# Optimization experiments

Measured on AMD Instinct MI355X. Metric: run time of the kernel, lower is better.

## Reference

```python
import jax, jax.numpy as jnp
import numpy as np

N_NODES = 100000
N_EDGES = 1600000
D = 128          # h_size == feature_representation_size
N_CLASSES = 2
N_GRAPHS = 64


def setup_inputs() -> dict:
    key = jax.random.key(0)
    ks = jax.random.split(key, 8)
    scale = 1.0 / np.sqrt(D)
    x = jax.random.normal(ks[0], (N_NODES, D), jnp.float32)
    edge_index = jax.random.randint(ks[1], (2, N_EDGES), 0, N_NODES, dtype=jnp.int64)
    batch = jnp.sort(jax.random.randint(ks[2], (N_NODES,), 0, N_GRAPHS, dtype=jnp.int64))
    W0 = jax.random.normal(ks[3], (D, D), jnp.float32) * scale
    W1 = jax.random.normal(ks[4], (D, D), jnp.float32) * scale
    W2 = jax.random.normal(ks[5], (D, D), jnp.float32) * scale
    Wf = jax.random.normal(ks[6], (D, N_CLASSES), jnp.float32) * scale
    return dict(
        x=x, edge_index=edge_index, batch=batch,
        W0=W0, b0=jnp.zeros((D,), jnp.float32),
        W1=W1, b1=jnp.zeros((D,), jnp.float32),
        W2=W2, b2=jnp.zeros((D,), jnp.float32),
        Wf=Wf, bf=jnp.zeros((N_CLASSES,), jnp.float32),
    )


def gcn_norm(edge_index, num_nodes):
    # add self loops, symmetric normalization D^{-1/2} A_hat D^{-1/2}
    src, dst = edge_index[0], edge_index[1]
    loop = jnp.arange(num_nodes, dtype=src.dtype)
    src = jnp.concatenate([src, loop])
    dst = jnp.concatenate([dst, loop])
    ew = jnp.ones(src.shape[0], jnp.float32)
    deg = jax.ops.segment_sum(ew, dst, num_segments=num_nodes)
    dinv = jnp.where(deg > 0, jax.lax.rsqrt(deg), 0.0)
    norm = dinv[src] * dinv[dst]  # [E+N]
    return src, dst, norm


def gcn_conv(h, W, b, src, dst, norm, num_nodes):
    h = h @ W                                   # linear transform
    msg = h[src] * norm[:, None]                # gather + scale over edges
    out = jax.ops.segment_sum(msg, dst, num_segments=num_nodes)  # scatter-add
    return out + b


def reference(x, edge_index, batch, W0, b0, W1, b1, W2, b2, Wf, bf):
    n = x.shape[0]
    src, dst, norm = gcn_norm(edge_index, n)
    h = jax.nn.relu(gcn_conv(x, W0, b0, src, dst, norm, n))
    h = jax.nn.relu(gcn_conv(h, W1, b1, src, dst, norm, n))
    h = gcn_conv(h, W2, b2, src, dst, norm, n)  # last layer, no relu
    pooled = jax.ops.segment_max(h, batch, num_segments=N_GRAPHS)  # global max pool
    return pooled @ Wf + bf
```

## Files before the change

### kernel.cpp

```cpp
#include <hip/hip_runtime.h>
#include <hip/hip_bf16.h>
#include <hip/hip_fp16.h>
#include <float.h>

#define D 128
#define NGRAPHS 64
#define BKSHIFT 9
#define BKNODES 512
#define MAXBK 256
#define PCH 2048

typedef _Float16 h8 __attribute__((ext_vector_type(8)));
typedef float f4 __attribute__((ext_vector_type(4)));

__device__ __forceinline__ unsigned fkey(float f){
  unsigned u = __float_as_uint(f);
  return (u & 0x80000000u) ? ~u : (u | 0x80000000u);
}
__device__ __forceinline__ float funkey(unsigned k){
  unsigned u = (k & 0x80000000u) ? (k ^ 0x80000000u) : ~k;
  return __uint_as_float(u);
}

__device__ __forceinline__ void wcvt_pair(const float* __restrict__ W,
    _Float16* __restrict__ dstp, int pair, int lane){
  int quad = lane >> 4;
  int n    = lane & 15;
  int k0 = pair >> 3;
  int tt = pair & 7;
  _Float16 v[8];
  #pragma unroll
  for (int j = 0; j < 8; j++){
    int k = k0 * 32 + quad * 8 + j;
    v[j] = (_Float16)W[k * 128 + 16 * tt + n];
  }
  *(uint4*)&dstp[((size_t)pair * 64 + lane) * 8] = *(uint4*)v;
}

__global__ __launch_bounds__(256) void k_wcvt0(const float* __restrict__ W0,
    _Float16* __restrict__ Wsw, int* __restrict__ bcnt){
  if (blockIdx.x == 0 && threadIdx.x < MAXBK) bcnt[threadIdx.x] = 0;
  int lane = threadIdx.x & 63;
  int pair = blockIdx.x * 4 + (threadIdx.x >> 6);
  wcvt_pair(W0, Wsw, pair, lane);
}

#define HCH 4096
__global__ __launch_bounds__(256) void k_mega(
    const float* __restrict__ x, const _Float16* __restrict__ Wsw0,
    _Float16* __restrict__ C, int M, int gb,
    const int* __restrict__ dst, int* __restrict__ bcnt, int E, int nh,
    const float* __restrict__ W1, const float* __restrict__ W2,
    _Float16* __restrict__ Wsw12){
  __shared__ __align__(16) char smraw[4 * 16 * 136 * 2];
  int bid = blockIdx.x;
  if (bid < gb){
    _Float16 (*lds)[136] = (_Float16(*)[136])(smraw + (threadIdx.x >> 6) * 16 * 136 * 2);
    int lane = threadIdx.x & 63;
    int quad = lane >> 4;
    int l15  = lane & 15;
    int m0 = bid * 64 + (threadIdx.x >> 6) * 16;
    if (m0 >= M) return;
    f4 acc[8] = {};
    h8 af[4];
    const float* arow = x + (size_t)(m0 + l15) * D;
    #pragma unroll
    for (int k0 = 0; k0 < 4; k0++){
      float4 a = *(const float4*)&arow[k0 * 32 + quad * 8];
      float4 b = *(const float4*)&arow[k0 * 32 + quad * 8 + 4];
      __half2 p0 = __floats2half2_rn(a.x, a.y);
      __half2 p1 = __floats2half2_rn(a.z, a.w);
      __half2 p2 = __floats2half2_rn(b.x, b.y);
      __half2 p3 = __floats2half2_rn(b.z, b.w);
      union { uint4 u; h8 v; } cv;
      cv.u.x = *(unsigned*)&p0; cv.u.y = *(unsigned*)&p1;
      cv.u.z = *(unsigned*)&p2; cv.u.w = *(unsigned*)&p3;
      af[k0] = cv.v;
    }
    #pragma unroll
    for (int k0 = 0; k0 < 4; k0++){
      #pragma unroll
      for (int t = 0; t < 8; t++){
        h8 bf = *(const h8*)&Wsw0[((size_t)(k0 * 8 + t) * 64 + lane) * 8];
        acc[t] = __builtin_amdgcn_mfma_f32_16x16x32_f16(af[k0], bf, acc[t], 0, 0, 0);
      }
    }
    #pragma unroll
    for (int t = 0; t < 8; t++){
      #pragma unroll
      for (int r = 0; r < 4; r++)
        lds[quad * 4 + r][t * 16 + l15] = (_Float16)acc[t][r];
    }
    #pragma unroll
    for (int it = 0; it < 4; it++){
      int idx = it * 64 + lane;
      int row = idx >> 4;
      int ch  = idx & 15;
      *(uint4*)&C[(size_t)(m0 + row) * D + ch * 8] = *(uint4*)&lds[row][ch * 8];
    }
    return;
  }
  bid -= gb;
  if (bid < nh){
    int* h = (int*)smraw;
    int t = threadIdx.x;
    for (int i = t; i < MAXBK; i += 256) h[i] = 0;
    __syncthreads();
    int e0 = bid * HCH;
    #pragma unroll
    for (int j = 0; j < HCH / 256; j++){
      int e = e0 + t + j * 256;
      if (e < E) atomicAdd(&h[dst[e] >> BKSHIFT], 1);
    }
    __syncthreads();
    for (int i = t; i < MAXBK; i += 256) if (h[i]) atomicAdd(&bcnt[i], h[i]);
    return;
  }
  bid -= nh;
  const float* W = (bid < 2) ? W1 : W2;
  _Float16* dstp = Wsw12 + ((bid < 2) ? 0 : 16384);
  int pbase = (bid & 1) * 16;
  int lane = threadIdx.x & 63;
  for (int pp = (threadIdx.x >> 6); pp < 16; pp += 4)
    wcvt_pair(W, dstp, pbase + pp, lane);
}

__global__ __launch_bounds__(256) void k_bscan(const int* __restrict__ bcnt,
    int* __restrict__ bOff, int* __restrict__ bCur, int* __restrict__ row_ptr,
    unsigned* __restrict__ pk, int nbk, int N, int E){
  __shared__ int sh[256];
  int t = threadIdx.x;
  for (int i = t; i < NGRAPHS * D; i += 256) pk[i] = 0u;
  int v = (t < nbk) ? bcnt[t] : 0;
  sh[t] = v; __syncthreads();
  for (int off = 1; off < 256; off <<= 1){
    int x = (t >= off) ? sh[t - off] : 0;
    __syncthreads();
    sh[t] += x;
    __syncthreads();
  }
  if (t < nbk){ int ex = sh[t] - v; bOff[t] = ex; bCur[t] = ex; }
  if (t == 0){ bOff[nbk] = E; row_ptr[N] = E; }
}

__global__ __launch_bounds__(256) void k_part(const int* __restrict__ src,
    const int* __restrict__ dst, int* __restrict__ bCur,
    uint2* __restrict__ epart, int E){
  __shared__ int scnt[MAXBK], soff[MAXBK], sbase[MAXBK], scur[MAXBK];
  __shared__ int stmp[256];
  __shared__ uint2 stage[PCH];
  int t = threadIdx.x;
  int e0 = blockIdx.x * PCH;
  int eN = E - e0; if (eN > PCH) eN = PCH;
  for (int i = t; i < MAXBK; i += 256){ scnt[i] = 0; scur[i] = 0; }
  __syncthreads();
  uint2 mye[PCH / 256];
  #pragma unroll
  for (int j = 0; j < PCH / 256; j++){
    int e = e0 + t + j * 256;
    if (e < E){
      mye[j].x = (unsigned)src[e];
      mye[j].y = (unsigned)dst[e];
      atomicAdd(&scnt[mye[j].y >> BKSHIFT], 1);
    }
  }
  __syncthreads();
  int v = scnt[t];
  stmp[t] = v; __syncthreads();
  for (int off = 1; off < 256; off <<= 1){
    int x = (t >= off) ? stmp[t - off] : 0;
    __syncthreads();
    stmp[t] += x;
    __syncthreads();
  }
  soff[t] = stmp[t] - v;
  if (v > 0) sbase[t] = atomicAdd(&bCur[t], v);
  __syncthreads();
  #pragma unroll
  for (int j = 0; j < PCH / 256; j++){
    int e = e0 + t + j * 256;
    if (e < E){
      int b = mye[j].y >> BKSHIFT;
      int l = atomicAdd(&scur[b], 1);
      stage[soff[b] + l] = mye[j];
    }
  }
  __syncthreads();
  for (int j = t; j < eN; j += 256){
    uint2 ed = stage[j];
    int b = (int)(ed.y >> BKSHIFT);
    epart[(size_t)sbase[b] + (j - soff[b])] = ed;
  }
}

__global__ __launch_bounds__(256) void k_bfill(const uint2* __restrict__ epart,
    const int* __restrict__ bOff, int* __restrict__ row_ptr,
    int* __restrict__ col, float* __restrict__ dinv, int N){
  __shared__ int hc[BKNODES], off[BKNODES], cur[BKNODES];
  __shared__ int stmp[256];
  int b = blockIdx.x, t = threadIdx.x;
  int base = bOff[b], cntE = bOff[b + 1] - base;
  int node0 = b << BKSHIFT;
  int nloc = N - node0; if (nloc > BKNODES) nloc = BKNODES;
  for (int i = t; i < BKNODES; i += 256) hc[i] = 0;
  __syncthreads();
  for (int j = t; j < cntE; j += 256){
    uint2 ed = epart[(size_t)base + j];
    atomicAdd(&hc[ed.y - node0], 1);
  }
  __syncthreads();
  int a0 = hc[2 * t], a1 = hc[2 * t + 1];
  int s = a0 + a1;
  stmp[t] = s; __syncthreads();
  for (int o = 1; o < 256; o <<= 1){
    int x = (t >= o) ? stmp[t - o] : 0;
    __syncthreads();
    stmp[t] += x;
    __syncthreads();
  }
  int ex = stmp[t] - s;
  off[2 * t] = ex; off[2 * t + 1] = ex + a0;
  __syncthreads();
  for (int i = t; i < nloc; i += 256){
    row_ptr[node0 + i] = base + off[i];
    dinv[node0 + i]    = rsqrtf((float)hc[i] + 1.0f);
    cur[i] = off[i];
  }
  __syncthreads();
  for (int j = t; j < cntE; j += 256){
    uint2 ed = epart[(size_t)base + j];
    int p = atomicAdd(&cur[ed.y - node0], 1);
    col[base + p] = (int)ed.x;
  }
}

__global__ __launch_bounds__(256) void gemm_mfma(const _Float16* __restrict__ A,
    const _Float16* __restrict__ Wsw, _Float16* __restrict__ C, int M){
  __shared__ _Float16 lds[4][16][136];
  int wave = threadIdx.x >> 6;
  int lane = threadIdx.x & 63;
  int quad = lane >> 4;
  int l15  = lane & 15;
  int m0 = blockIdx.x * 64 + wave * 16;
  if (m0 >= M) return;
  f4 acc[8] = {};
  h8 af[4];
  const _Float16* arow = A + (size_t)(m0 + l15) * D;
  #pragma unroll
  for (int k0 = 0; k0 < 4; k0++)
    af[k0] = *(const h8*)&arow[k0 * 32 + quad * 8];
  #pragma unroll
  for (int k0 = 0; k0 < 4; k0++){
    #pragma unroll
    for (int t = 0; t < 8; t++){
      h8 bf = *(const h8*)&Wsw[((size_t)(k0 * 8 + t) * 64 + lane) * 8];
      acc[t] = __builtin_amdgcn_mfma_f32_16x16x32_f16(af[k0], bf, acc[t], 0, 0, 0);
    }
  }
  #pragma unroll
  for (int t = 0; t < 8; t++){
    #pragma unroll
    for (int r = 0; r < 4; r++)
      lds[wave][quad * 4 + r][t * 16 + l15] = (_Float16)acc[t][r];
  }
  #pragma unroll
  for (int it = 0; it < 4; it++){
    int idx = it * 64 + lane;
    int row = idx >> 4;
    int ch  = idx & 15;
    *(uint4*)&C[(size_t)(m0 + row) * D + ch * 8] = *(uint4*)&lds[wave][row][ch * 8];
  }
}

__device__ __forceinline__ void accm(float* acc, uint4 u, float w){
  union { uint4 u; _Float16 h[8]; } cv;
  cv.u = u;
  #pragma unroll
  for (int k = 0; k < 8; k++)
    acc[k] += (float)cv.h[k] * w;
}

__global__ __launch_bounds__(256) void k_agg(const __half* __restrict__ t,
    const int* __restrict__ row_ptr, const int* __restrict__ col,
    const float* __restrict__ dinv, const float* __restrict__ bias,
    __half* __restrict__ outh, int relu, int N){
  int node = blockIdx.x * 4 + (threadIdx.x >> 6);
  if (node >= N) return;
  int lane = threadIdx.x & 63;
  int way  = lane >> 4;
  int cg   = (lane & 15) * 8;
  float di = dinv[node];
  int beg = row_ptr[node], end = row_ptr[node + 1];
  float acc[8] = {0.f,0.f,0.f,0.f,0.f,0.f,0.f,0.f};
  int j = beg + way;
  for (; j + 12 < end; j += 16){
    int s0 = col[j], s1 = col[j + 4], s2 = col[j + 8], s3 = col[j + 12];
    float w0 = dinv[s0] * di;
    float w1 = dinv[s1] * di;
    float w2 = dinv[s2] * di;
    float w3 = dinv[s3] * di;
    uint4 u0 = *(const uint4*)&t[(size_t)s0 * D + cg];
    uint4 u1 = *(const uint4*)&t[(size_t)s1 * D + cg];
    uint4 u2 = *(const uint4*)&t[(size_t)s2 * D + cg];
    uint4 u3 = *(const uint4*)&t[(size_t)s3 * D + cg];
    accm(acc, u0, w0);
    accm(acc, u1, w1);
    accm(acc, u2, w2);
    accm(acc, u3, w3);
  }
  for (; j < end; j += 4){
    int s = col[j];
    float w = dinv[s] * di;
    uint4 u = *(const uint4*)&t[(size_t)s * D + cg];
    accm(acc, u, w);
  }
  #pragma unroll
  for (int k = 0; k < 8; k++){
    acc[k] += __shfl_xor(acc[k], 16, 64);
    acc[k] += __shfl_xor(acc[k], 32, 64);
  }
  if (way == 0){
    uint4 su = *(const uint4*)&t[(size_t)node * D + cg];
    union { uint4 u; _Float16 h[8]; } sv; sv.u = su;
    float dii = di * di;
    float4 b0 = *(const float4*)&bias[cg];
    float4 b1 = *(const float4*)&bias[cg + 4];
    float bb[8] = {b0.x, b0.y, b0.z, b0.w, b1.x, b1.y, b1.z, b1.w};
    float o[8];
    #pragma unroll
    for (int k = 0; k < 8; k++)
      o[k] = acc[k] + (float)sv.h[k] * dii + bb[k];
    if (relu){
      #pragma unroll
      for (int k = 0; k < 8; k++) o[k] = fmaxf(o[k], 0.f);
    }
    __half2 p0 = __floats2half2_rn(o[0], o[1]);
    __half2 p1 = __floats2half2_rn(o[2], o[3]);
    __half2 p2 = __floats2half2_rn(o[4], o[5]);
    __half2 p3 = __floats2half2_rn(o[6], o[7]);
    uint4 u;
    u.x = *(unsigned*)&p0; u.y = *(unsigned*)&p1;
    u.z = *(unsigned*)&p2; u.w = *(unsigned*)&p3;
    *(uint4*)&outh[(size_t)node * D + cg] = u;
  }
}

__global__ __launch_bounds__(128) void k_pool(const __half* __restrict__ h,
    const int* __restrict__ batch, unsigned* __restrict__ pk, int N){
  int d = threadIdx.x;
  int n0 = blockIdx.x * 64;
  int nEnd = n0 + 64; if (nEnd > N) nEnd = N;
  float cur = -FLT_MAX;
  int curg = batch[n0];
  int n = n0;
  for (; n + 3 < nEnd; n += 4){
    const __half* r = &h[(size_t)n * D + d];
    __half v0 = r[0], v1 = r[D], v2 = r[2 * D], v3 = r[3 * D];
    int g0 = batch[n], g1 = batch[n + 1], g2 = batch[n + 2], g3 = batch[n + 3];
    if (g0 != curg){ atomicMax(&pk[curg * D + d], fkey(cur)); cur = -FLT_MAX; curg = g0; }
    cur = fmaxf(cur, __half2float(v0));
    if (g1 != curg){ atomicMax(&pk[curg * D + d], fkey(cur)); cur = -FLT_MAX; curg = g1; }
    cur = fmaxf(cur, __half2float(v1));
    if (g2 != curg){ atomicMax(&pk[curg * D + d], fkey(cur)); cur = -FLT_MAX; curg = g2; }
    cur = fmaxf(cur, __half2float(v2));
    if (g3 != curg){ atomicMax(&pk[curg * D + d], fkey(cur)); cur = -FLT_MAX; curg = g3; }
    cur = fmaxf(cur, __half2float(v3));
  }
  for (; n < nEnd; n++){
    int g = batch[n];
    if (g != curg){ atomicMax(&pk[curg * D + d], fkey(cur)); cur = -FLT_MAX; curg = g; }
    cur = fmaxf(cur, __half2float(h[(size_t)n * D + d]));
  }
  atomicMax(&pk[curg * D + d], fkey(cur));
}

__global__ __launch_bounds__(128) void k_final(const unsigned* __restrict__ pk,
    const float* __restrict__ Wf, const float* __restrict__ bf,
    float* __restrict__ out){
  int t = threadIdx.x;
  int g = t >> 1, c = t & 1;
  float s = bf[c];
  for (int k = 0; k < D; k++)
    s += funkey(pk[g * D + k]) * Wf[k * 2 + c];
  out[g * 2 + c] = s;
}

extern "C" void kernel_launch(void* const* d_in, const int* in_sizes, int n_in,
                              void* d_out, int out_size, void* d_ws, size_t ws_size,
                              hipStream_t stream){
  const float* x   = (const float*)d_in[0];
  const int*   ei  = (const int*)d_in[1];
  const int*   bat = (const int*)d_in[2];
  const float* W0  = (const float*)d_in[3];
  const float* b0  = (const float*)d_in[4];
  const float* W1  = (const float*)d_in[5];
  const float* b1  = (const float*)d_in[6];
  const float* W2  = (const float*)d_in[7];
  const float* b2  = (const float*)d_in[8];
  const float* Wf  = (const float*)d_in[9];
  const float* bf  = (const float*)d_in[10];
  int N = in_sizes[0] / D;
  int E = in_sizes[1] / 2;
  const int* srcp = ei;
  const int* dstp = ei + E;
  int nbk   = (N + BKNODES - 1) / BKNODES;
  int npart = (E + PCH - 1) / PCH;
  int nh    = (E + HCH - 1) / HCH;
  int gb    = (N + 63) / 64;

  char* p = (char*)d_ws;
  auto alloc = [&](size_t bytes)->char*{
    char* r = p; p += (bytes + 255) & ~(size_t)255; return r;
  };
  float*     dinv    = (float*)alloc((size_t)N * 4);
  int*       row_ptr = (int*)alloc((size_t)(N + 1) * 4);
  int*       col     = (int*)alloc((size_t)E * 4);
  uint2*     epart   = (uint2*)alloc((size_t)E * 8);
  _Float16*  tmp     = (_Float16*)alloc((size_t)N * D * 2);
  _Float16*  tmp2    = (_Float16*)alloc((size_t)N * D * 2);
  _Float16*  Wsw     = (_Float16*)alloc((size_t)3 * 16384 * 2);
  unsigned*  pk      = (unsigned*)alloc((size_t)NGRAPHS * D * 4);
  int*       bcnt    = (int*)alloc((size_t)MAXBK * 4);
  int*       bOff    = (int*)alloc((size_t)(MAXBK + 1) * 4);
  int*       bCur    = (int*)alloc((size_t)MAXBK * 4);

  k_wcvt0<<<8, 256, 0, stream>>>(W0, Wsw, bcnt);
  k_mega<<<gb + nh + 4, 256, 0, stream>>>(x, Wsw, tmp, N, gb,
      dstp, bcnt, E, nh, W1, W2, Wsw + 16384);
  k_bscan<<<1, 256, 0, stream>>>(bcnt, bOff, bCur, row_ptr, pk, nbk, N, E);
  k_part<<<npart, 256, 0, stream>>>(srcp, dstp, bCur, epart, E);
  k_bfill<<<nbk, 256, 0, stream>>>(epart, bOff, row_ptr, col, dinv, N);

  int ablocks = (N + 3) / 4;
  k_agg<<<ablocks, 256, 0, stream>>>((const __half*)tmp, row_ptr, col, dinv, b0, (__half*)tmp2, 1, N);
  gemm_mfma<<<gb, 256, 0, stream>>>(tmp2, Wsw + 16384, tmp, N);
  k_agg<<<ablocks, 256, 0, stream>>>((const __half*)tmp, row_ptr, col, dinv, b1, (__half*)tmp2, 1, N);
  gemm_mfma<<<gb, 256, 0, stream>>>(tmp2, Wsw + 32768, tmp, N);
  k_agg<<<ablocks, 256, 0, stream>>>((const __half*)tmp, row_ptr, col, dinv, b2, (__half*)tmp2, 0, N);
  k_pool<<<(N + 63) / 64, 128, 0, stream>>>((const __half*)tmp2, bat, pk, N);
  k_final<<<1, 128, 0, stream>>>(pk, Wf, bf, (float*)d_out);
}
```

Measured before the change: 408.8 us.

## Fuse edge partition with first GEMM and pack partitioned edges into 32 bits

The histogram is split out into its own kernel, and the edge-partition pass is merged into the big fused kernel alongside the first-layer GEMM and the W1/W2 conversion, so partitioning overlaps with the GEMM. Partitioned edges are now stored as one 32-bit word (9-bit local dst plus 23-bit src) instead of a uint2, halving epart traffic in the partition and fill kernels. The cost is a larger union shared-memory footprint for the GEMM blocks, which may reduce their occupancy, and the packing requires fewer than 2^23 nodes.

```diff
diff --git a/kernel.cpp b/kernel.cpp
--- a/kernel.cpp
+++ b/kernel.cpp
@@ -9,6 +9,7 @@
 #define BKNODES 512
 #define MAXBK 256
 #define PCH 2048
+#define HCH 4096
 
 typedef _Float16 h8 __attribute__((ext_vector_type(8)));
 typedef float f4 __attribute__((ext_vector_type(4)));
@@ -45,17 +46,103 @@
   wcvt_pair(W0, Wsw, pair, lane);
 }
 
-#define HCH 4096
-__global__ __launch_bounds__(256) void k_mega(
+__global__ __launch_bounds__(256) void k_hist(const int* __restrict__ dst,
+    int* __restrict__ bcnt, int E){
+  __shared__ int h[MAXBK];
+  int t = threadIdx.x;
+  for (int i = t; i < MAXBK; i += 256) h[i] = 0;
+  __syncthreads();
+  int e0 = blockIdx.x * HCH;
+  #pragma unroll
+  for (int j = 0; j < HCH / 256; j++){
+    int e = e0 + t + j * 256;
+    if (e < E) atomicAdd(&h[dst[e] >> BKSHIFT], 1);
+  }
+  __syncthreads();
+  for (int i = t; i < MAXBK; i += 256) if (h[i]) atomicAdd(&bcnt[i], h[i]);
+}
+
+__global__ __launch_bounds__(256) void k_bscan(const int* __restrict__ bcnt,
+    int* __restrict__ bOff, int* __restrict__ bCur, int* __restrict__ row_ptr,
+    unsigned* __restrict__ pk, int nbk, int N, int E){
+  __shared__ int sh[256];
+  int t = threadIdx.x;
+  for (int i = t; i < NGRAPHS * D; i += 256) pk[i] = 0u;
+  int v = (t < nbk) ? bcnt[t] : 0;
+  sh[t] = v; __syncthreads();
+  for (int off = 1; off < 256; off <<= 1){
+    int x = (t >= off) ? sh[t - off] : 0;
+    __syncthreads();
+    sh[t] += x;
+    __syncthreads();
+  }
+  if (t < nbk){ int ex = sh[t] - v; bOff[t] = ex; bCur[t] = ex; }
+  if (t == 0){ bOff[nbk] = E; row_ptr[N] = E; }
+}
+
+__global__ __launch_bounds__(256) void k_mega2(
+    const int* __restrict__ srce, const int* __restrict__ dste,
+    int* __restrict__ bCur, unsigned* __restrict__ epart, int E, int npart,
     const float* __restrict__ x, const _Float16* __restrict__ Wsw0,
     _Float16* __restrict__ C, int M, int gb,
-    const int* __restrict__ dst, int* __restrict__ bcnt, int E, int nh,
     const float* __restrict__ W1, const float* __restrict__ W2,
     _Float16* __restrict__ Wsw12){
-  __shared__ __align__(16) char smraw[4 * 16 * 136 * 2];
+  union SM {
+    struct { int scnt[MAXBK]; int soff[MAXBK]; int sbase[MAXBK];
+             int scur[MAXBK]; int stmp[256]; uint2 stage[PCH]; } p;
+    _Float16 g[4][16][136];
+  };
+  __shared__ SM sm;
   int bid = blockIdx.x;
+  if (bid < npart){
+    int t = threadIdx.x;
+    int e0 = bid * PCH;
+    int eN = E - e0; if (eN > PCH) eN = PCH;
+    for (int i = t; i < MAXBK; i += 256){ sm.p.scnt[i] = 0; sm.p.scur[i] = 0; }
+    __syncthreads();
+    uint2 mye[PCH / 256];
+    #pragma unroll
+    for (int j = 0; j < PCH / 256; j++){
+      int e = e0 + t + j * 256;
+      if (e < E){
+        mye[j].x = (unsigned)srce[e];
+        mye[j].y = (unsigned)dste[e];
+        atomicAdd(&sm.p.scnt[mye[j].y >> BKSHIFT], 1);
+      }
+    }
+    __syncthreads();
+    int v = sm.p.scnt[t];
+    sm.p.stmp[t] = v; __syncthreads();
+    for (int off = 1; off < 256; off <<= 1){
+      int xx = (t >= off) ? sm.p.stmp[t - off] : 0;
+      __syncthreads();
+      sm.p.stmp[t] += xx;
+      __syncthreads();
+    }
+    sm.p.soff[t] = sm.p.stmp[t] - v;
+    if (v > 0) sm.p.sbase[t] = atomicAdd(&bCur[t], v);
+    __syncthreads();
+    #pragma unroll
+    for (int j = 0; j < PCH / 256; j++){
+      int e = e0 + t + j * 256;
+      if (e < E){
+        int b = mye[j].y >> BKSHIFT;
+        int l = atomicAdd(&sm.p.scur[b], 1);
+        sm.p.stage[sm.p.soff[b] + l] = mye[j];
+      }
+    }
+    __syncthreads();
+    for (int j = t; j < eN; j += 256){
+      uint2 ed = sm.p.stage[j];
+      int b = (int)(ed.y >> BKSHIFT);
+      epart[(size_t)sm.p.sbase[b] + (j - sm.p.soff[b])] =
+          ((ed.y & (BKNODES - 1)) << 23) | ed.x;
+    }
+    return;
+  }
+  bid -= npart;
   if (bid < gb){
-    _Float16 (*lds)[136] = (_Float16(*)[136])(smraw + (threadIdx.x >> 6) * 16 * 136 * 2);
+    _Float16 (*lds)[136] = sm.g[threadIdx.x >> 6];
     int lane = threadIdx.x & 63;
     int quad = lane >> 4;
     int l15  = lane & 15;
@@ -101,22 +188,6 @@
     return;
   }
   bid -= gb;
-  if (bid < nh){
-    int* h = (int*)smraw;
-    int t = threadIdx.x;
-    for (int i = t; i < MAXBK; i += 256) h[i] = 0;
-    __syncthreads();
-    int e0 = bid * HCH;
-    #pragma unroll
-    for (int j = 0; j < HCH / 256; j++){
-      int e = e0 + t + j * 256;
-      if (e < E) atomicAdd(&h[dst[e] >> BKSHIFT], 1);
-    }
-    __syncthreads();
-    for (int i = t; i < MAXBK; i += 256) if (h[i]) atomicAdd(&bcnt[i], h[i]);
-    return;
-  }
-  bid -= nh;
   const float* W = (bid < 2) ? W1 : W2;
   _Float16* dstp = Wsw12 + ((bid < 2) ? 0 : 16384);
   int pbase = (bid & 1) * 16;
@@ -125,75 +196,7 @@
     wcvt_pair(W, dstp, pbase + pp, lane);
 }
 
-__global__ __launch_bounds__(256) void k_bscan(const int* __restrict__ bcnt,
-    int* __restrict__ bOff, int* __restrict__ bCur, int* __restrict__ row_ptr,
-    unsigned* __restrict__ pk, int nbk, int N, int E){
-  __shared__ int sh[256];
-  int t = threadIdx.x;
-  for (int i = t; i < NGRAPHS * D; i += 256) pk[i] = 0u;
-  int v = (t < nbk) ? bcnt[t] : 0;
-  sh[t] = v; __syncthreads();
-  for (int off = 1; off < 256; off <<= 1){
-    int x = (t >= off) ? sh[t - off] : 0;
-    __syncthreads();
-    sh[t] += x;
-    __syncthreads();
-  }
-  if (t < nbk){ int ex = sh[t] - v; bOff[t] = ex; bCur[t] = ex; }
-  if (t == 0){ bOff[nbk] = E; row_ptr[N] = E; }
-}
-
-__global__ __launch_bounds__(256) void k_part(const int* __restrict__ src,
-    const int* __restrict__ dst, int* __restrict__ bCur,
-    uint2* __restrict__ epart, int E){
-  __shared__ int scnt[MAXBK], soff[MAXBK], sbase[MAXBK], scur[MAXBK];
-  __shared__ int stmp[256];
-  __shared__ uint2 stage[PCH];
-  int t = threadIdx.x;
-  int e0 = blockIdx.x * PCH;
-  int eN = E - e0; if (eN > PCH) eN = PCH;
-  for (int i = t; i < MAXBK; i += 256){ scnt[i] = 0; scur[i] = 0; }
-  __syncthreads();
-  uint2 mye[PCH / 256];
-  #pragma unroll
-  for (int j = 0; j < PCH / 256; j++){
-    int e = e0 + t + j * 256;
-    if (e < E){
-      mye[j].x = (unsigned)src[e];
-      mye[j].y = (unsigned)dst[e];
-      atomicAdd(&scnt[mye[j].y >> BKSHIFT], 1);
-    }
-  }
-  __syncthreads();
-  int v = scnt[t];
-  stmp[t] = v; __syncthreads();
-  for (int off = 1; off < 256; off <<= 1){
-    int x = (t >= off) ? stmp[t - off] : 0;
-    __syncthreads();
-    stmp[t] += x;
-    __syncthreads();
-  }
-  soff[t] = stmp[t] - v;
-  if (v > 0) sbase[t] = atomicAdd(&bCur[t], v);
-  __syncthreads();
-  #pragma unroll
-  for (int j = 0; j < PCH / 256; j++){
-    int e = e0 + t + j * 256;
-    if (e < E){
-      int b = mye[j].y >> BKSHIFT;
-      int l = atomicAdd(&scur[b], 1);
-      stage[soff[b] + l] = mye[j];
-    }
-  }
-  __syncthreads();
-  for (int j = t; j < eN; j += 256){
-    uint2 ed = stage[j];
-    int b = (int)(ed.y >> BKSHIFT);
-    epart[(size_t)sbase[b] + (j - soff[b])] = ed;
-  }
-}
-
-__global__ __launch_bounds__(256) void k_bfill(const uint2* __restrict__ epart,
+__global__ __launch_bounds__(256) void k_bfill(const unsigned* __restrict__ epart,
     const int* __restrict__ bOff, int* __restrict__ row_ptr,
     int* __restrict__ col, float* __restrict__ dinv, int N){
   __shared__ int hc[BKNODES], off[BKNODES], cur[BKNODES];
@@ -205,8 +208,8 @@
   for (int i = t; i < BKNODES; i += 256) hc[i] = 0;
   __syncthreads();
   for (int j = t; j < cntE; j += 256){
-    uint2 ed = epart[(size_t)base + j];
-    atomicAdd(&hc[ed.y - node0], 1);
+    unsigned ed = epart[(size_t)base + j];
+    atomicAdd(&hc[ed >> 23], 1);
   }
   __syncthreads();
   int a0 = hc[2 * t], a1 = hc[2 * t + 1];
@@ -228,9 +231,9 @@
   }
   __syncthreads();
   for (int j = t; j < cntE; j += 256){
-    uint2 ed = epart[(size_t)base + j];
-    int p = atomicAdd(&cur[ed.y - node0], 1);
-    col[base + p] = (int)ed.x;
+    unsigned ed = epart[(size_t)base + j];
+    int p = atomicAdd(&cur[ed >> 23], 1);
+    col[base + p] = (int)(ed & 0x7FFFFFu);
   }
 }
 
@@ -415,7 +418,7 @@
   float*     dinv    = (float*)alloc((size_t)N * 4);
   int*       row_ptr = (int*)alloc((size_t)(N + 1) * 4);
   int*       col     = (int*)alloc((size_t)E * 4);
-  uint2*     epart   = (uint2*)alloc((size_t)E * 8);
+  unsigned*  epart   = (unsigned*)alloc((size_t)E * 4);
   _Float16*  tmp     = (_Float16*)alloc((size_t)N * D * 2);
   _Float16*  tmp2    = (_Float16*)alloc((size_t)N * D * 2);
   _Float16*  Wsw     = (_Float16*)alloc((size_t)3 * 16384 * 2);
@@ -425,10 +428,10 @@
   int*       bCur    = (int*)alloc((size_t)MAXBK * 4);
 
   k_wcvt0<<<8, 256, 0, stream>>>(W0, Wsw, bcnt);
-  k_mega<<<gb + nh + 4, 256, 0, stream>>>(x, Wsw, tmp, N, gb,
-      dstp, bcnt, E, nh, W1, W2, Wsw + 16384);
+  k_hist<<<nh, 256, 0, stream>>>(dstp, bcnt, E);
   k_bscan<<<1, 256, 0, stream>>>(bcnt, bOff, bCur, row_ptr, pk, nbk, N, E);
-  k_part<<<npart, 256, 0, stream>>>(srcp, dstp, bCur, epart, E);
+  k_mega2<<<npart + gb + 4, 256, 0, stream>>>(srcp, dstp, bCur, epart, E, npart,
+      x, Wsw, tmp, N, gb, W1, W2, Wsw + 16384);
   k_bfill<<<nbk, 256, 0, stream>>>(epart, bOff, row_ptr, col, dinv, N);
 
   int ablocks = (N + 3) / 4;
```

Result: no change. 412.0 us (+0.8%).
